# Optimization experiments

Measured on AMD Instinct MI355X. Metric: run time of the kernel, lower is better.

The kernel has to match this reference:

```python
import jax, jax.numpy as jnp
import numpy as np

N_NODES = 100000
N_GRAPHS = 64


def gcn_conv(x, src, dst, W, b, num_nodes):
    """PyG GCNConv: add self-loops, symmetric deg normalization, aggregate at dst."""
    h = x @ W  # [N, out]
    ones_e = jnp.ones(src.shape[0], dtype=x.dtype)
    # degree includes self-loop (+1)
    deg = jax.ops.segment_sum(ones_e, dst, num_segments=num_nodes) + 1.0
    dinv = jnp.where(deg > 0, 1.0 / jnp.sqrt(deg), 0.0)  # deg>=1 always here
    norm = dinv[src] * dinv[dst]  # [E]
    msg = h[src] * norm[:, None]  # gather + scale
    agg = jax.ops.segment_sum(msg, dst, num_segments=num_nodes)
    # self-loop contribution: norm_ii = dinv[i]^2
    agg = agg + h * (dinv * dinv)[:, None]
    return agg + b


def global_mean_pool(x, batch, num_graphs):
    sums = jax.ops.segment_sum(x, batch, num_segments=num_graphs)
    counts = jax.ops.segment_sum(jnp.ones(x.shape[0], dtype=x.dtype), batch,
                                 num_segments=num_graphs)
    return sums / jnp.maximum(counts, 1.0)[:, None]


def setup_inputs() -> dict:
    key = jax.random.key(0)
    ks = jax.random.split(key, 8)
    H = 128
    x = jax.random.normal(ks[0], (N_NODES, 4), dtype=jnp.float32)
    edge_index = jax.random.randint(ks[1], (2, 1600000), 0, N_NODES, dtype=jnp.int64 if jax.config.read('jax_enable_x64') else jnp.int32)
    batch = jnp.sort(jax.random.randint(ks[2], (N_NODES,), 0, N_GRAPHS))
    def glorot(k, shape):
        fan_in, fan_out = shape
        lim = np.sqrt(6.0 / (fan_in + fan_out))
        return jax.random.uniform(k, shape, jnp.float32, -lim, lim)
    return {
        'x': x,
        'edge_index': edge_index,
        'batch': batch,
        'W1': glorot(ks[3], (4, H)), 'b1': jnp.zeros((H,), jnp.float32),
        'W2': glorot(ks[4], (H, H)), 'b2': jnp.zeros((H,), jnp.float32),
        'W3': glorot(ks[5], (H, H)), 'b3': jnp.zeros((H,), jnp.float32),
        'Wl': glorot(ks[6], (H, 2)), 'bl': jnp.zeros((2,), jnp.float32),
    }


def reference(x, edge_index, batch, W1, b1, W2, b2, W3, b3, Wl, bl):
    src, dst = edge_index[0], edge_index[1]
    h = jax.nn.relu(gcn_conv(x, src, dst, W1, b1, N_NODES))
    h = jax.nn.relu(gcn_conv(h, src, dst, W2, b2, N_NODES))
    h = jax.nn.relu(gcn_conv(h, src, dst, W3, b3, N_NODES))
    g = global_mean_pool(h, batch, N_GRAPHS)  # [G, H]
    logits = g @ Wl + bl  # [G, 2]
    return jax.nn.log_softmax(logits, axis=1)
```

## Files before the change

### kernel.cpp

```cpp
#include <hip/hip_runtime.h>

#define HDIM 128
#define NGRAPH 64

#define BSHIFT 9
#define NBUCK 196
#define BCAP 64
#define BSTR 65
#define RCAP 9216
#define BIN_CHUNK 4096

typedef __attribute__((ext_vector_type(8))) short short8;
typedef __attribute__((ext_vector_type(4))) float floatx4;
typedef __attribute__((ext_vector_type(2))) float floatx2;

__device__ __forceinline__ float bf2f(unsigned short u) {
    union { unsigned int i; float f; } v;
    v.i = ((unsigned int)u) << 16;
    return v.f;
}
__device__ __forceinline__ unsigned short f2bf(float f) {
    unsigned int u = __float_as_uint(f);
    u += 0x7FFFu + ((u >> 16) & 1u);
    return (unsigned short)(u >> 16);
}

__global__ __launch_bounds__(256) void k_misc(int* __restrict__ gcur,
                                              const int* __restrict__ batch,
                                              float* __restrict__ gcnt,
                                              float* __restrict__ gsum,
                                              const float* __restrict__ W2,
                                              unsigned short* __restrict__ Wp2,
                                              const float* __restrict__ W3,
                                              unsigned short* __restrict__ Wp3,
                                              int N, int nbuck) {
    int t = threadIdx.x;
    int blk = blockIdx.x;
    if (blk == 0) {
        if (t < nbuck) gcur[t] = t * RCAP;
        for (int i = t; i < NGRAPH * 128; i += 256) gsum[i] = 0.f;
        if (t < NGRAPH) {
            int g = t;
            int lo = 0, hi = N;
            while (lo < hi) { int m = (lo + hi) >> 1; if (batch[m] < g) lo = m + 1; else hi = m; }
            int lb = lo;
            lo = 0; hi = N;
            while (lo < hi) { int m = (lo + hi) >> 1; if (batch[m] < g + 1) lo = m + 1; else hi = m; }
            gcnt[g] = (float)(lo - lb);
        }
        return;
    }
    const float* W = (blk <= 64) ? W2 : W3;
    unsigned short* Wp = (blk <= 64) ? Wp2 : Wp3;
    int idx = ((blk <= 64) ? (blk - 1) : (blk - 65)) * 256 + t;
    int j = idx & 7, l = (idx >> 3) & 63, frag = idx >> 9;
    int c = frag >> 2, ks = frag & 3;
    int k = ks * 32 + ((l >> 4) & 3) * 8 + j;
    int n = c * 16 + (l & 15);
    Wp[idx] = f2bf(W[k * 128 + n]);
}


__global__ __launch_bounds__(256) void k_binA(const int* __restrict__ src,
                                              const int* __restrict__ dst,
                                              int* __restrict__ gcur,
                                              unsigned int* __restrict__ binned, int E) {
    __shared__ unsigned int bin[NBUCK * BSTR];
    __shared__ int bcnt[NBUCK];
    __shared__ int bbase[NBUCK];
    int t = threadIdx.x;
    for (int b = t; b < NBUCK; b += 256) bcnt[b] = 0;
    __syncthreads();
    int e0 = blockIdx.x * BIN_CHUNK;
    #pragma unroll
    for (int i = 0; i < BIN_CHUNK / 1024; i++) {
        int e = e0 + i * 1024 + t * 4;
        if (e + 3 < E) {
            const int4 d4 = *(const int4*)&dst[e];
            const int4 s4 = *(const int4*)&src[e];
            int dd[4] = {d4.x, d4.y, d4.z, d4.w};
            int ss[4] = {s4.x, s4.y, s4.z, s4.w};
            #pragma unroll
            for (int k = 0; k < 4; k++) {
                int d = dd[k];
                unsigned int rec = ((unsigned int)(d & 511) << 20) | (unsigned int)ss[k];
                int b = d >> BSHIFT;
                int idx = atomicAdd(&bcnt[b], 1);
                if (idx < BCAP) bin[b * BSTR + idx] = rec;
                else { int p = atomicAdd(&gcur[b], 1); binned[p] = rec; }
            }
        } else {
            for (int k = 0; k < 4; k++) {
                int e2 = e + k;
                if (e2 < E) {
                    int d = dst[e2];
                    unsigned int rec = ((unsigned int)(d & 511) << 20) | (unsigned int)src[e2];
                    int b = d >> BSHIFT;
                    int idx = atomicAdd(&bcnt[b], 1);
                    if (idx < BCAP) bin[b * BSTR + idx] = rec;
                    else { int p = atomicAdd(&gcur[b], 1); binned[p] = rec; }
                }
            }
        }
    }
    __syncthreads();
    if (t < NBUCK) {
        int cnt = min(bcnt[t], BCAP);
        bbase[t] = atomicAdd(&gcur[t], cnt);
    }
    __syncthreads();
    int wave = t >> 6, lane = t & 63;
    for (int b = wave; b < NBUCK; b += 4) {
        int cnt = min(bcnt[b], BCAP);
        int base = bbase[b];
        if (lane < cnt) binned[base + lane] = bin[b * BSTR + lane];
    }
}

__global__ __launch_bounds__(256) void k_fillB(const int* __restrict__ gcur,
                                               const unsigned int* __restrict__ binned,
                                               int* __restrict__ P,
                                               float* __restrict__ dinv,
                                               int* __restrict__ csr, int N, int nbuck) {
    __shared__ int ps[256];
    __shared__ int cnt[512];
    __shared__ int image[RCAP];
    int b = blockIdx.x;
    int t = threadIdx.x;
    int lt = (t < nbuck) ? (gcur[t] - t * RCAP) : 0;
    ps[t] = lt;
    __syncthreads();
    for (int d = 1; d < 256; d <<= 1) {
        int o = (t >= d) ? ps[t - d] : 0;
        __syncthreads();
        ps[t] += o;
        __syncthreads();
    }
    int start = (b > 0) ? ps[b - 1] : 0;
    int len = ps[b] - start;
    __syncthreads();

    int n0 = b << BSHIFT;
    int nloc = min(n0 + 512, N) - n0;
    cnt[t] = 0; cnt[t + 256] = 0;
    __syncthreads();
    const unsigned int* rb = binned + (size_t)b * RCAP;
    for (int i = t; i < len; i += 256) atomicAdd(&cnt[rb[i] >> 20], 1);
    __syncthreads();
    int c0 = cnt[2 * t], c1 = cnt[2 * t + 1];
    int pair = c0 + c1;
    __syncthreads();
    cnt[t] = pair;
    __syncthreads();
    for (int d = 1; d < 256; d <<= 1) {
        int o = (t >= d) ? cnt[t - d] : 0;
        __syncthreads();
        cnt[t] += o;
        __syncthreads();
    }
    int excl = cnt[t] - pair;
    __syncthreads();
    if (2 * t < nloc) {
        P[n0 + 2 * t] = start + excl;
        dinv[n0 + 2 * t] = rsqrtf((float)c0 + 1.0f);
    }
    if (2 * t + 1 < nloc) {
        P[n0 + 2 * t + 1] = start + excl + c0;
        dinv[n0 + 2 * t + 1] = rsqrtf((float)c1 + 1.0f);
    }
    if (b == nbuck - 1 && t == 0) P[N] = start + len;
    cnt[2 * t] = excl;
    cnt[2 * t + 1] = excl + c0;
    __syncthreads();
    for (int i = t; i < len; i += 256) {
        unsigned int rec = rb[i];
        int pos = atomicAdd(&cnt[rec >> 20], 1);
        image[pos] = (int)(rec & 0xFFFFFu);
    }
    __syncthreads();
    for (int i = t; i < len; i += 256) csr[start + i] = image[i];
}

__global__ void k_aggx_csr(const int* __restrict__ P, const int* __restrict__ csr,
                           const float4* __restrict__ x, const float* __restrict__ dinv,
                           float4* __restrict__ aggx, int N) {
    int d = blockIdx.x * blockDim.x + threadIdx.x;
    if (d >= N) return;
    int s0 = P[d], s1 = P[d + 1];
    float dd = dinv[d];
    float4 xv = x[d];
    float4 a = make_float4(xv.x * dd, xv.y * dd, xv.z * dd, xv.w * dd);
    int i = s0;
    int pre = min(s1, (s0 + 3) & ~3);
    for (; i < pre; i++) {
        int s = csr[i];
        float4 v = x[s];
        float ds = dinv[s];
        a.x += v.x * ds; a.y += v.y * ds; a.z += v.z * ds; a.w += v.w * ds;
    }
    for (; i + 8 <= s1; i += 8) {
        const int4 iA = *(const int4*)&csr[i];
        const int4 iB = *(const int4*)&csr[i + 4];
        float4 vA = x[iA.x], vB = x[iA.y], vC = x[iA.z], vD = x[iA.w];
        float4 vE = x[iB.x], vF = x[iB.y], vG = x[iB.z], vH = x[iB.w];
        float dA = dinv[iA.x], dB = dinv[iA.y], dC = dinv[iA.z], dD = dinv[iA.w];
        float dE = dinv[iB.x], dF = dinv[iB.y], dG = dinv[iB.z], dH = dinv[iB.w];
        a.x += vA.x * dA + vB.x * dB + vC.x * dC + vD.x * dD
             + vE.x * dE + vF.x * dF + vG.x * dG + vH.x * dH;
        a.y += vA.y * dA + vB.y * dB + vC.y * dC + vD.y * dD
             + vE.y * dE + vF.y * dF + vG.y * dG + vH.y * dH;
        a.z += vA.z * dA + vB.z * dB + vC.z * dC + vD.z * dD
             + vE.z * dE + vF.z * dF + vG.z * dG + vH.z * dH;
        a.w += vA.w * dA + vB.w * dB + vC.w * dC + vD.w * dD
             + vE.w * dE + vF.w * dF + vG.w * dG + vH.w * dH;
    }
    for (; i + 4 <= s1; i += 4) {
        const int4 ix = *(const int4*)&csr[i];
        float4 vA = x[ix.x], vB = x[ix.y], vC = x[ix.z], vD = x[ix.w];
        float dA = dinv[ix.x], dB = dinv[ix.y], dC = dinv[ix.z], dD = dinv[ix.w];
        a.x += vA.x * dA + vB.x * dB + vC.x * dC + vD.x * dD;
        a.y += vA.y * dA + vB.y * dB + vC.y * dC + vD.y * dD;
        a.z += vA.z * dA + vB.z * dB + vC.z * dC + vD.z * dD;
        a.w += vA.w * dA + vB.w * dB + vC.w * dC + vD.w * dD;
    }
    for (; i < s1; i++) {
        int s = csr[i];
        float4 v = x[s];
        float ds = dinv[s];
        a.x += v.x * ds; a.y += v.y * ds; a.z += v.z * ds; a.w += v.w * ds;
    }
    aggx[d] = make_float4(a.x * dd, a.y * dd, a.z * dd, a.w * dd);
}

#define LXS 136
__global__ __launch_bounds__(256) void k_l1t2(const float4* __restrict__ aggx,
                                              const float* __restrict__ W1,
                                              const float* __restrict__ b1,
                                              const unsigned short* __restrict__ Wp,
                                              const float* __restrict__ dinv,
                                              unsigned char* __restrict__ out8, int N) {
    __shared__ unsigned short lx[64 * LXS];
    __shared__ unsigned short lw[16384];
    __shared__ float w1s[512];
    __shared__ float b1s[128];
    __shared__ float ax[64][4];
    int t = threadIdx.x;
    int n0 = blockIdx.x * 64;

    for (int i = t; i < 512; i += 256) w1s[i] = W1[i];
    if (t < 128) b1s[t] = b1[t];
    if (t < 64) {
        float4 v = (n0 + t < N) ? aggx[n0 + t] : make_float4(0.f, 0.f, 0.f, 0.f);
        ax[t][0] = v.x; ax[t][1] = v.y; ax[t][2] = v.z; ax[t][3] = v.w;
    }
    for (int ch = t; ch < 2048; ch += 256)
        *(uint4*)&lw[ch * 8] = *(const uint4*)&Wp[ch * 8];
    __syncthreads();

    for (int i = t; i < 8192; i += 256) {
        int n = i >> 7, j = i & 127;
        float v = b1s[j] + ax[n][0] * w1s[j] + ax[n][1] * w1s[128 + j]
                         + ax[n][2] * w1s[256 + j] + ax[n][3] * w1s[384 + j];
        lx[n * LXS + j] = f2bf(fmaxf(v, 0.f));
    }
    __syncthreads();

    int w = t >> 6, lane = t & 63;
    int m0 = w * 16;
    int col = lane & 15, quad = lane >> 4;

    short8 afrag[4];
    #pragma unroll
    for (int ks = 0; ks < 4; ks++)
        afrag[ks] = *(const short8*)&lx[(m0 + col) * LXS + ks * 32 + quad * 8];

    float dv[4];
    #pragma unroll
    for (int r = 0; r < 4; r++) {
        int gn = n0 + m0 + quad * 4 + r;
        dv[r] = (gn < N) ? dinv[gn] : 0.0f;
    }

    #pragma unroll
    for (int c = 0; c < 8; c++) {
        floatx4 acc = {0.f, 0.f, 0.f, 0.f};
        #pragma unroll
        for (int ks = 0; ks < 4; ks++) {
            const short8 bfrag = *(const short8*)&lw[((c * 4 + ks) * 64 + lane) * 8];
            acc = __builtin_amdgcn_mfma_f32_16x16x32_bf16(afrag[ks], bfrag, acc, 0, 0, 0);
        }
        #pragma unroll
        for (int r = 0; r < 4; r++) {
            int gn = n0 + m0 + quad * 4 + r;
            if (gn < N) {
                float v = acc[r] * dv[r];
                out8[(size_t)gn * 128 + c * 16 + col] =
                    (unsigned char)(__builtin_amdgcn_cvt_pk_fp8_f32(v, v, 0, false) & 0xFF);
            }
        }
    }
}

__global__ __launch_bounds__(256) void k_transform_mfma(const unsigned short* __restrict__ in,
                                                        const unsigned short* __restrict__ Wp,
                                                        const float* __restrict__ dinv,
                                                        unsigned char* __restrict__ out8, int N) {
    __shared__ unsigned short lx[64 * LXS];
    __shared__ unsigned short lw[16384];
    int t = threadIdx.x;
    int n0 = blockIdx.x * 64;

    for (int ch = t; ch < 1024; ch += 256) {
        int row = ch >> 4, part = ch & 15;
        uint4 val = make_uint4(0, 0, 0, 0);
        if (n0 + row < N) val = *(const uint4*)&in[(size_t)(n0 + row) * 128 + part * 8];
        *(uint4*)&lx[row * LXS + part * 8] = val;
    }
    for (int ch = t; ch < 2048; ch += 256)
        *(uint4*)&lw[ch * 8] = *(const uint4*)&Wp[ch * 8];
    __syncthreads();

    int w = t >> 6, lane = t & 63;
    int m0 = w * 16;
    int col = lane & 15, quad = lane >> 4;

    short8 afrag[4];
    #pragma unroll
    for (int ks = 0; ks < 4; ks++)
        afrag[ks] = *(const short8*)&lx[(m0 + col) * LXS + ks * 32 + quad * 8];

    float dv[4];
    #pragma unroll
    for (int r = 0; r < 4; r++) {
        int gn = n0 + m0 + quad * 4 + r;
        dv[r] = (gn < N) ? dinv[gn] : 0.0f;
    }

    #pragma unroll
    for (int c = 0; c < 8; c++) {
        floatx4 acc = {0.f, 0.f, 0.f, 0.f};
        #pragma unroll
        for (int ks = 0; ks < 4; ks++) {
            const short8 bfrag = *(const short8*)&lw[((c * 4 + ks) * 64 + lane) * 8];
            acc = __builtin_amdgcn_mfma_f32_16x16x32_bf16(afrag[ks], bfrag, acc, 0, 0, 0);
        }
        #pragma unroll
        for (int r = 0; r < 4; r++) {
            int gn = n0 + m0 + quad * 4 + r;
            if (gn < N) {
                float v = acc[r] * dv[r];
                out8[(size_t)gn * 128 + c * 16 + col] =
                    (unsigned char)(__builtin_amdgcn_cvt_pk_fp8_f32(v, v, 0, false) & 0xFF);
            }
        }
    }
}

__device__ __forceinline__ void fp8acc(unsigned int u, float& a0, float& a1,
                                       float& a2, float& a3) {
    floatx2 lo = __builtin_amdgcn_cvt_pk_f32_fp8(u, false);
    floatx2 hi = __builtin_amdgcn_cvt_pk_f32_fp8(u, true);
    a0 += lo.x; a1 += lo.y; a2 += hi.x; a3 += hi.y;
}

__device__ __forceinline__ void gather_fp8(const int* __restrict__ csr,
                                           const unsigned int* __restrict__ hs8,
                                           int s0, int s1, int lane,
                                           float& a0, float& a1, float& a2, float& a3) {
    int i = s0;
    int pre = min(s1, (s0 + 3) & ~3);
    for (; i < pre; i++)
        fp8acc(hs8[(size_t)csr[i] * 32 + lane], a0, a1, a2, a3);
    for (; i + 8 <= s1; i += 8) {
        const int4 iA = *(const int4*)&csr[i];
        const int4 iB = *(const int4*)&csr[i + 4];
        unsigned int u0 = hs8[(size_t)iA.x * 32 + lane];
        unsigned int u1 = hs8[(size_t)iA.y * 32 + lane];
        unsigned int u2 = hs8[(size_t)iA.z * 32 + lane];
        unsigned int u3 = hs8[(size_t)iA.w * 32 + lane];
        unsigned int u4 = hs8[(size_t)iB.x * 32 + lane];
        unsigned int u5 = hs8[(size_t)iB.y * 32 + lane];
        unsigned int u6 = hs8[(size_t)iB.z * 32 + lane];
        unsigned int u7 = hs8[(size_t)iB.w * 32 + lane];
        fp8acc(u0, a0, a1, a2, a3); fp8acc(u1, a0, a1, a2, a3);
        fp8acc(u2, a0, a1, a2, a3); fp8acc(u3, a0, a1, a2, a3);
        fp8acc(u4, a0, a1, a2, a3); fp8acc(u5, a0, a1, a2, a3);
        fp8acc(u6, a0, a1, a2, a3); fp8acc(u7, a0, a1, a2, a3);
    }
    for (; i + 4 <= s1; i += 4) {
        const int4 iA = *(const int4*)&csr[i];
        unsigned int u0 = hs8[(size_t)iA.x * 32 + lane];
        unsigned int u1 = hs8[(size_t)iA.y * 32 + lane];
        unsigned int u2 = hs8[(size_t)iA.z * 32 + lane];
        unsigned int u3 = hs8[(size_t)iA.w * 32 + lane];
        fp8acc(u0, a0, a1, a2, a3); fp8acc(u1, a0, a1, a2, a3);
        fp8acc(u2, a0, a1, a2, a3); fp8acc(u3, a0, a1, a2, a3);
    }
    for (; i < s1; i++)
        fp8acc(hs8[(size_t)csr[i] * 32 + lane], a0, a1, a2, a3);
}

__global__ __launch_bounds__(256) void k_agg_csr(const int* __restrict__ P,
                                                 const int* __restrict__ csr,
                                                 const unsigned int* __restrict__ hs8,
                                                 const float* __restrict__ dinv,
                                                 const float* __restrict__ bias,
                                                 unsigned short* __restrict__ out, int N) {
    int g = (blockIdx.x * 256 + threadIdx.x) >> 5;
    int lane = threadIdx.x & 31;
    if (g >= N) return;
    int s0 = P[g], s1 = P[g + 1];
    unsigned int su = hs8[(size_t)g * 32 + lane];
    floatx2 slo = __builtin_amdgcn_cvt_pk_f32_fp8(su, false);
    floatx2 shi = __builtin_amdgcn_cvt_pk_f32_fp8(su, true);
    float a0 = slo.x, a1 = slo.y, a2 = shi.x, a3 = shi.y;
    gather_fp8(csr, hs8, s0, s1, lane, a0, a1, a2, a3);
    float dd = dinv[g];
    const float4 bb = *(const float4*)&bias[lane * 4];
    ushort4 o;
    o.x = f2bf(fmaxf(a0 * dd + bb.x, 0.f));
    o.y = f2bf(fmaxf(a1 * dd + bb.y, 0.f));
    o.z = f2bf(fmaxf(a2 * dd + bb.z, 0.f));
    o.w = f2bf(fmaxf(a3 * dd + bb.w, 0.f));
    *(ushort4*)&out[(size_t)g * 128 + lane * 4] = o;
}

#define POOL_ROWS 64
__global__ __launch_bounds__(128) void k_pool(const unsigned short* __restrict__ h,
                                              const int* __restrict__ batch,
                                              float* __restrict__ gsum, int N) {
    int n0 = blockIdx.x * POOL_ROWS;
    if (n0 >= N) return;
    int len = min(POOL_ROWS, N - n0);
    int j = threadIdx.x;
    int bFirst = batch[n0];
    int bLast = batch[n0 + len - 1];
    if (bFirst == bLast) {
        float acc = 0.f;
        #pragma unroll 8
        for (int i = 0; i < len; i++) acc += bf2f(h[(size_t)(n0 + i) * 128 + j]);
        unsafeAtomicAdd(&gsum[(size_t)bFirst * 128 + j], acc);
    } else {
        float acc = 0.f;
        int cur = bFirst;
        for (int i = 0; i < len; i++) {
            int b = batch[n0 + i];
            if (b != cur) {
                unsafeAtomicAdd(&gsum[(size_t)cur * 128 + j], acc);
                acc = 0.f; cur = b;
            }
            acc += bf2f(h[(size_t)(n0 + i) * 128 + j]);
        }
        unsafeAtomicAdd(&gsum[(size_t)cur * 128 + j], acc);
    }
}

__global__ __launch_bounds__(256) void k_head(const float* __restrict__ gsum,
                                              const float* __restrict__ gcnt,
                                              const float* __restrict__ Wl,
                                              const float* __restrict__ bl,
                                              float* __restrict__ out, int G) {
    int t = threadIdx.x;
    int g = t >> 2, q = t & 3;
    if (g >= G) return;
    float l0 = 0.f, l1 = 0.f;
    #pragma unroll
    for (int k = 0; k < 32; k++) {
        int jj = q * 32 + k;
        float v = gsum[(size_t)g * 128 + jj];
        l0 += v * Wl[jj * 2 + 0];
        l1 += v * Wl[jj * 2 + 1];
    }
    l0 += __shfl_xor(l0, 1, 64); l1 += __shfl_xor(l1, 1, 64);
    l0 += __shfl_xor(l0, 2, 64); l1 += __shfl_xor(l1, 2, 64);
    if (q == 0) {
        float inv = 1.0f / fmaxf(gcnt[g], 1.0f);
        l0 = l0 * inv + bl[0];
        l1 = l1 * inv + bl[1];
        float m = fmaxf(l0, l1);
        float lse = m + logf(expf(l0 - m) + expf(l1 - m));
        out[g * 2 + 0] = l0 - lse;
        out[g * 2 + 1] = l1 - lse;
    }
}


extern "C" void kernel_launch(void* const* d_in, const int* in_sizes, int n_in,
                              void* d_out, int out_size, void* d_ws, size_t ws_size,
                              hipStream_t stream) {
    const float* x   = (const float*)d_in[0];
    const int*   ei  = (const int*)d_in[1];
    const int*   bat = (const int*)d_in[2];
    const float* W1  = (const float*)d_in[3];
    const float* b1  = (const float*)d_in[4];
    const float* W2  = (const float*)d_in[5];
    const float* b2  = (const float*)d_in[6];
    const float* W3  = (const float*)d_in[7];
    const float* b3  = (const float*)d_in[8];
    const float* Wl  = (const float*)d_in[9];
    const float* bl  = (const float*)d_in[10];

    const int N = in_sizes[0] / 4;
    const int E = in_sizes[1] / 2;
    const int* srcI = ei;
    const int* dstI = ei + E;

    const int nbuck = (N + 511) >> BSHIFT;
    const int pAlloc = ((N + 1 + 3) & ~3) + 4;

    float* wsf  = (float*)d_ws;
    float* dinv = wsf;
    int*   P    = (int*)(dinv + N);
    int*   csr  = P + pAlloc;
    float* aggx = (float*)(csr + E);
    unsigned short* bufA16 = (unsigned short*)(aggx + (size_t)N * 4);
    unsigned char*  hs8    = (unsigned char*)(bufA16 + (size_t)N * 128);
    unsigned short* Wp2    = (unsigned short*)(hs8 + (size_t)N * 128);
    unsigned short* Wp3    = Wp2 + 16384;
    float* gsum = (float*)(Wp3 + 16384);
    float* gcnt = gsum + NGRAPH * 128;
    int*   gcur = (int*)(gcnt + NGRAPH);
    unsigned int* binned = (unsigned int*)hs8;

    k_misc<<<129, 256, 0, stream>>>(gcur, bat, gcnt, gsum, W2, Wp2, W3, Wp3, N, nbuck);
    k_binA<<<(E + BIN_CHUNK - 1) / BIN_CHUNK, 256, 0, stream>>>(srcI, dstI, gcur, binned, E);
    k_fillB<<<nbuck, 256, 0, stream>>>(gcur, binned, P, dinv, csr, N, nbuck);

    k_aggx_csr<<<(N + 255) / 256, 256, 0, stream>>>(P, csr, (const float4*)x, dinv,
                                                    (float4*)aggx, N);
    k_l1t2<<<(N + 63) / 64, 256, 0, stream>>>((const float4*)aggx, W1, b1, Wp2, dinv, hs8, N);

    k_agg_csr<<<(N * 32 + 255) / 256, 256, 0, stream>>>(P, csr, (const unsigned int*)hs8,
                                                        dinv, b2, bufA16, N);

    k_transform_mfma<<<(N + 63) / 64, 256, 0, stream>>>(bufA16, Wp3, dinv, hs8, N);
    k_agg_csr<<<(N * 32 + 255) / 256, 256, 0, stream>>>(P, csr, (const unsigned int*)hs8,
                                                        dinv, b3, bufA16, N);

    k_pool<<<(N + POOL_ROWS - 1) / POOL_ROWS, 128, 0, stream>>>(bufA16, bat, gsum, N);
    k_head<<<1, 256, 0, stream>>>(gsum, gcnt, Wl, bl, (float*)d_out, NGRAPH);
}
```

Measured before the change: 328.1 us.

## Aggregate two nodes per warp group and store layer-3 output as FP8

Replaces the single-node CSR aggregation with a kernel where each 32-lane group processes two destination nodes in interleaved 4-edge steps. This raises the number of independent gathers in flight per group. Lanes pad the shorter node's neighbour list with masked loads of row 0, which wastes some bandwidth when the two degrees differ. The final layer now writes FP8 instead of BF16, and the pooling kernel reads FP8 bytes, cutting write and read traffic at a small accuracy risk in the pooled means.

```diff
diff --git a/kernel.cpp b/kernel.cpp
--- a/kernel.cpp
+++ b/kernel.cpp
@@ -363,72 +363,104 @@
     a0 += lo.x; a1 += lo.y; a2 += hi.x; a3 += hi.y;
 }
 
-__device__ __forceinline__ void gather_fp8(const int* __restrict__ csr,
-                                           const unsigned int* __restrict__ hs8,
-                                           int s0, int s1, int lane,
-                                           float& a0, float& a1, float& a2, float& a3) {
-    int i = s0;
-    int pre = min(s1, (s0 + 3) & ~3);
-    for (; i < pre; i++)
-        fp8acc(hs8[(size_t)csr[i] * 32 + lane], a0, a1, a2, a3);
-    for (; i + 8 <= s1; i += 8) {
-        const int4 iA = *(const int4*)&csr[i];
-        const int4 iB = *(const int4*)&csr[i + 4];
-        unsigned int u0 = hs8[(size_t)iA.x * 32 + lane];
-        unsigned int u1 = hs8[(size_t)iA.y * 32 + lane];
-        unsigned int u2 = hs8[(size_t)iA.z * 32 + lane];
-        unsigned int u3 = hs8[(size_t)iA.w * 32 + lane];
-        unsigned int u4 = hs8[(size_t)iB.x * 32 + lane];
-        unsigned int u5 = hs8[(size_t)iB.y * 32 + lane];
-        unsigned int u6 = hs8[(size_t)iB.z * 32 + lane];
-        unsigned int u7 = hs8[(size_t)iB.w * 32 + lane];
-        fp8acc(u0, a0, a1, a2, a3); fp8acc(u1, a0, a1, a2, a3);
-        fp8acc(u2, a0, a1, a2, a3); fp8acc(u3, a0, a1, a2, a3);
-        fp8acc(u4, a0, a1, a2, a3); fp8acc(u5, a0, a1, a2, a3);
-        fp8acc(u6, a0, a1, a2, a3); fp8acc(u7, a0, a1, a2, a3);
-    }
-    for (; i + 4 <= s1; i += 4) {
-        const int4 iA = *(const int4*)&csr[i];
-        unsigned int u0 = hs8[(size_t)iA.x * 32 + lane];
-        unsigned int u1 = hs8[(size_t)iA.y * 32 + lane];
-        unsigned int u2 = hs8[(size_t)iA.z * 32 + lane];
-        unsigned int u3 = hs8[(size_t)iA.w * 32 + lane];
-        fp8acc(u0, a0, a1, a2, a3); fp8acc(u1, a0, a1, a2, a3);
-        fp8acc(u2, a0, a1, a2, a3); fp8acc(u3, a0, a1, a2, a3);
-    }
-    for (; i < s1; i++)
-        fp8acc(hs8[(size_t)csr[i] * 32 + lane], a0, a1, a2, a3);
-}
-
-__global__ __launch_bounds__(256) void k_agg_csr(const int* __restrict__ P,
-                                                 const int* __restrict__ csr,
-                                                 const unsigned int* __restrict__ hs8,
-                                                 const float* __restrict__ dinv,
-                                                 const float* __restrict__ bias,
-                                                 unsigned short* __restrict__ out, int N) {
-    int g = (blockIdx.x * 256 + threadIdx.x) >> 5;
+__global__ __launch_bounds__(256) void k_agg_dual(const int* __restrict__ P,
+                                                  const int* __restrict__ csr,
+                                                  const unsigned int* __restrict__ hs8,
+                                                  const float* __restrict__ dinv,
+                                                  const float* __restrict__ bias,
+                                                  unsigned short* __restrict__ out16,
+                                                  unsigned int* __restrict__ out8,
+                                                  int N, int write8) {
+    int grp = (blockIdx.x * 256 + threadIdx.x) >> 5;
     int lane = threadIdx.x & 31;
-    if (g >= N) return;
-    int s0 = P[g], s1 = P[g + 1];
-    unsigned int su = hs8[(size_t)g * 32 + lane];
-    floatx2 slo = __builtin_amdgcn_cvt_pk_f32_fp8(su, false);
-    floatx2 shi = __builtin_amdgcn_cvt_pk_f32_fp8(su, true);
-    float a0 = slo.x, a1 = slo.y, a2 = shi.x, a3 = shi.y;
-    gather_fp8(csr, hs8, s0, s1, lane, a0, a1, a2, a3);
-    float dd = dinv[g];
+    int gA = grp * 2, gB = gA + 1;
+    if (gA >= N) return;
+    bool hasB = (gB < N);
+    int s0A = P[gA], s1A = P[gA + 1];
+    int s0B = hasB ? P[gB] : 0;
+    int s1B = hasB ? P[gB + 1] : 0;
+    int lenA = s1A - s0A, lenB = s1B - s0B;
+
+    unsigned int suA = hs8[(size_t)gA * 32 + lane];
+    float a0 = 0.f, a1 = 0.f, a2 = 0.f, a3 = 0.f;
+    fp8acc(suA, a0, a1, a2, a3);
+    float b0 = 0.f, b1v = 0.f, b2 = 0.f, b3 = 0.f;
+    if (hasB) {
+        unsigned int suB = hs8[(size_t)gB * 32 + lane];
+        fp8acc(suB, b0, b1v, b2, b3);
+    }
+
+    int len = max(lenA, lenB);
+    for (int i = 0; i < len; i += 4) {
+        int eA0 = (i + 0 < lenA) ? csr[s0A + i + 0] : 0;
+        int eA1 = (i + 1 < lenA) ? csr[s0A + i + 1] : 0;
+        int eA2 = (i + 2 < lenA) ? csr[s0A + i + 2] : 0;
+        int eA3 = (i + 3 < lenA) ? csr[s0A + i + 3] : 0;
+        int eB0 = (i + 0 < lenB) ? csr[s0B + i + 0] : 0;
+        int eB1 = (i + 1 < lenB) ? csr[s0B + i + 1] : 0;
+        int eB2 = (i + 2 < lenB) ? csr[s0B + i + 2] : 0;
+        int eB3 = (i + 3 < lenB) ? csr[s0B + i + 3] : 0;
+        unsigned int uA0 = hs8[(size_t)eA0 * 32 + lane];
+        unsigned int uA1 = hs8[(size_t)eA1 * 32 + lane];
+        unsigned int uA2 = hs8[(size_t)eA2 * 32 + lane];
+        unsigned int uA3 = hs8[(size_t)eA3 * 32 + lane];
+        unsigned int uB0 = hs8[(size_t)eB0 * 32 + lane];
+        unsigned int uB1 = hs8[(size_t)eB1 * 32 + lane];
+        unsigned int uB2 = hs8[(size_t)eB2 * 32 + lane];
+        unsigned int uB3 = hs8[(size_t)eB3 * 32 + lane];
+        uA0 = (i + 0 < lenA) ? uA0 : 0u;
+        uA1 = (i + 1 < lenA) ? uA1 : 0u;
+        uA2 = (i + 2 < lenA) ? uA2 : 0u;
+        uA3 = (i + 3 < lenA) ? uA3 : 0u;
+        uB0 = (i + 0 < lenB) ? uB0 : 0u;
+        uB1 = (i + 1 < lenB) ? uB1 : 0u;
+        uB2 = (i + 2 < lenB) ? uB2 : 0u;
+        uB3 = (i + 3 < lenB) ? uB3 : 0u;
+        fp8acc(uA0, a0, a1, a2, a3); fp8acc(uA1, a0, a1, a2, a3);
+        fp8acc(uA2, a0, a1, a2, a3); fp8acc(uA3, a0, a1, a2, a3);
+        fp8acc(uB0, b0, b1v, b2, b3); fp8acc(uB1, b0, b1v, b2, b3);
+        fp8acc(uB2, b0, b1v, b2, b3); fp8acc(uB3, b0, b1v, b2, b3);
+    }
+
     const float4 bb = *(const float4*)&bias[lane * 4];
-    ushort4 o;
-    o.x = f2bf(fmaxf(a0 * dd + bb.x, 0.f));
-    o.y = f2bf(fmaxf(a1 * dd + bb.y, 0.f));
-    o.z = f2bf(fmaxf(a2 * dd + bb.z, 0.f));
-    o.w = f2bf(fmaxf(a3 * dd + bb.w, 0.f));
-    *(ushort4*)&out[(size_t)g * 128 + lane * 4] = o;
+    {
+        float dd = dinv[gA];
+        float o0 = fmaxf(a0 * dd + bb.x, 0.f);
+        float o1 = fmaxf(a1 * dd + bb.y, 0.f);
+        float o2 = fmaxf(a2 * dd + bb.z, 0.f);
+        float o3 = fmaxf(a3 * dd + bb.w, 0.f);
+        if (write8) {
+            unsigned int wv = __builtin_amdgcn_cvt_pk_fp8_f32(o0, o1, 0, false);
+            wv = __builtin_amdgcn_cvt_pk_fp8_f32(o2, o3, wv, true);
+            out8[(size_t)gA * 32 + lane] = wv;
+        } else {
+            ushort4 o;
+            o.x = f2bf(o0); o.y = f2bf(o1); o.z = f2bf(o2); o.w = f2bf(o3);
+            *(ushort4*)&out16[(size_t)gA * 128 + lane * 4] = o;
+        }
+    }
+    if (hasB) {
+        float dd = dinv[gB];
+        float o0 = fmaxf(b0 * dd + bb.x, 0.f);
+        float o1 = fmaxf(b1v * dd + bb.y, 0.f);
+        float o2 = fmaxf(b2 * dd + bb.z, 0.f);
+        float o3 = fmaxf(b3 * dd + bb.w, 0.f);
+        if (write8) {
+            unsigned int wv = __builtin_amdgcn_cvt_pk_fp8_f32(o0, o1, 0, false);
+            wv = __builtin_amdgcn_cvt_pk_fp8_f32(o2, o3, wv, true);
+            out8[(size_t)gB * 32 + lane] = wv;
+        } else {
+            ushort4 o;
+            o.x = f2bf(o0); o.y = f2bf(o1); o.z = f2bf(o2); o.w = f2bf(o3);
+            *(ushort4*)&out16[(size_t)gB * 128 + lane * 4] = o;
+        }
+    }
 }
 
 #define POOL_ROWS 64
-__global__ __launch_bounds__(128) void k_pool(const unsigned short* __restrict__ h,
-                                              const int* __restrict__ batch,
-                                              float* __restrict__ gsum, int N) {
+__global__ __launch_bounds__(128) void k_pool8(const unsigned char* __restrict__ h8,
+                                               const int* __restrict__ batch,
+                                               float* __restrict__ gsum, int N) {
     int n0 = blockIdx.x * POOL_ROWS;
     if (n0 >= N) return;
     int len = min(POOL_ROWS, N - n0);
@@ -438,7 +470,11 @@
     if (bFirst == bLast) {
         float acc = 0.f;
         #pragma unroll 8
-        for (int i = 0; i < len; i++) acc += bf2f(h[(size_t)(n0 + i) * 128 + j]);
+        for (int i = 0; i < len; i++) {
+            unsigned int u = h8[(size_t)(n0 + i) * 128 + j];
+            floatx2 lo = __builtin_amdgcn_cvt_pk_f32_fp8(u, false);
+            acc += lo.x;
+        }
         unsafeAtomicAdd(&gsum[(size_t)bFirst * 128 + j], acc);
     } else {
         float acc = 0.f;
@@ -449,7 +485,9 @@
                 unsafeAtomicAdd(&gsum[(size_t)cur * 128 + j], acc);
                 acc = 0.f; cur = b;
             }
-            acc += bf2f(h[(size_t)(n0 + i) * 128 + j]);
+            unsigned int u = h8[(size_t)(n0 + i) * 128 + j];
+            floatx2 lo = __builtin_amdgcn_cvt_pk_f32_fp8(u, false);
+            acc += lo.x;
         }
         unsafeAtomicAdd(&gsum[(size_t)cur * 128 + j], acc);
     }
@@ -521,6 +559,7 @@
     float* gcnt = gsum + NGRAPH * 128;
     int*   gcur = (int*)(gcnt + NGRAPH);
     unsigned int* binned = (unsigned int*)hs8;
+    unsigned char* h3f8  = (unsigned char*)bufA16;
 
     k_misc<<<129, 256, 0, stream>>>(gcur, bat, gcnt, gsum, W2, Wp2, W3, Wp3, N, nbuck);
     k_binA<<<(E + BIN_CHUNK - 1) / BIN_CHUNK, 256, 0, stream>>>(srcI, dstI, gcur, binned, E);
@@ -530,13 +569,15 @@
                                                     (float4*)aggx, N);
     k_l1t2<<<(N + 63) / 64, 256, 0, stream>>>((const float4*)aggx, W1, b1, Wp2, dinv, hs8, N);
 
-    k_agg_csr<<<(N * 32 + 255) / 256, 256, 0, stream>>>(P, csr, (const unsigned int*)hs8,
-                                                        dinv, b2, bufA16, N);
+    const int npair = (N + 1) / 2;
+    const int aggBlocks = (npair * 32 + 255) / 256;
+    k_agg_dual<<<aggBlocks, 256, 0, stream>>>(P, csr, (const unsigned int*)hs8, dinv, b2,
+                                              bufA16, nullptr, N, 0);
 
     k_transform_mfma<<<(N + 63) / 64, 256, 0, stream>>>(bufA16, Wp3, dinv, hs8, N);
-    k_agg_csr<<<(N * 32 + 255) / 256, 256, 0, stream>>>(P, csr, (const unsigned int*)hs8,
-                                                        dinv, b3, bufA16, N);
-
-    k_pool<<<(N + POOL_ROWS - 1) / POOL_ROWS, 128, 0, stream>>>(bufA16, bat, gsum, N);
+    k_agg_dual<<<aggBlocks, 256, 0, stream>>>(P, csr, (const unsigned int*)hs8, dinv, b3,
+                                              nullptr, (unsigned int*)h3f8, N, 1);
+
+    k_pool8<<<(N + POOL_ROWS - 1) / POOL_ROWS, 128, 0, stream>>>(h3f8, bat, gsum, N);
     k_head<<<1, 256, 0, stream>>>(gsum, gcnt, Wl, bl, (float*)d_out, NGRAPH);
 }
```

After: 352.3 us. 7.4% more time.
